# Performance work log

Hardware: AMD Instinct MI355X
Metric: run time of the kernel (lower is better)

Reference implementation:

```python
import jax, jax.numpy as jnp
import numpy as np

EPS = 1e-12  # matches torch F.normalize default eps

def setup_inputs() -> dict:
    key = jax.random.key(0)
    k1, k2 = jax.random.split(key)
    pred = jax.random.normal(k1, (32768, 2, 1024), dtype=jnp.float32)
    gt = jax.random.normal(k2, (32768, 2, 1024), dtype=jnp.float32)
    return {"pred": pred, "gt": gt}

def _l2_normalize(x):
    norm = jnp.sqrt(jnp.sum(x * x, axis=-1, keepdims=True))
    return x / jnp.maximum(norm, EPS)

def reference(pred, gt):
    # pred, gt: [B, 2, D]
    p = _l2_normalize(pred)
    g = _l2_normalize(gt)
    # cos: [B, 2, 2] cosine-similarity matrix between slots
    cos = jnp.einsum('bid,bjd->bij', p, g)
    # Hungarian assignment over a 2x2 cost (-cos) reduces to choosing the
    # larger of trace vs anti-trace of cos.
    s_id = cos[:, 0, 0] + cos[:, 1, 1]    # identity assignment sum
    s_sw = cos[:, 0, 1] + cos[:, 1, 0]    # swapped assignment sum
    # selection is done on detached values in the original (scipy on .detach())
    pick_id = jax.lax.stop_gradient(s_id >= s_sw)
    best_sum = jnp.where(pick_id, s_id, s_sw)
    loss_b = 1.0 - best_sum / 2.0          # 1 - mean of the 2 matched sims
    return jnp.mean(loss_b)
```

## Files before the change

kernel.cpp:

```cpp
#include <hip/hip_runtime.h>

#define NROWS 32768
#define DDIM 1024
#define ROWS_PER_BLOCK 16
#define ROWS_PER_WAVE 4

static __device__ __forceinline__ float dot4(float4 a, float4 b) {
    return a.x * b.x + a.y * b.y + a.z * b.z + a.w * b.w;
}

__global__ __launch_bounds__(256) void cosloss_main(const float* __restrict__ pred,
                                                    const float* __restrict__ gt,
                                                    float* __restrict__ partial) {
    const int wave = threadIdx.x >> 6;
    const int lane = threadIdx.x & 63;
    __shared__ float s_wave[4];

    float wave_best = 0.0f;
    const int row0 = blockIdx.x * ROWS_PER_BLOCK + wave * ROWS_PER_WAVE;

    for (int r = 0; r < ROWS_PER_WAVE; ++r) {
        const int row = row0 + r;
        const float4* pp = (const float4*)(pred + (size_t)row * (2 * DDIM));
        const float4* gg = (const float4*)(gt + (size_t)row * (2 * DDIM));

        float np0 = 0.f, np1 = 0.f, ng0 = 0.f, ng1 = 0.f;
        float d00 = 0.f, d01 = 0.f, d10 = 0.f, d11 = 0.f;

        #pragma unroll
        for (int k = 0; k < 4; ++k) {
            const int idx = k * 64 + lane;
            float4 a0 = pp[idx];
            float4 a1 = pp[idx + 256];
            float4 b0 = gg[idx];
            float4 b1 = gg[idx + 256];
            np0 += dot4(a0, a0);
            np1 += dot4(a1, a1);
            ng0 += dot4(b0, b0);
            ng1 += dot4(b1, b1);
            d00 += dot4(a0, b0);
            d01 += dot4(a0, b1);
            d10 += dot4(a1, b0);
            d11 += dot4(a1, b1);
        }

        #pragma unroll
        for (int off = 32; off; off >>= 1) {
            np0 += __shfl_xor(np0, off);
            np1 += __shfl_xor(np1, off);
            ng0 += __shfl_xor(ng0, off);
            ng1 += __shfl_xor(ng1, off);
            d00 += __shfl_xor(d00, off);
            d01 += __shfl_xor(d01, off);
            d10 += __shfl_xor(d10, off);
            d11 += __shfl_xor(d11, off);
        }

        if (lane == 0) {
            const float EPS = 1e-12f;
            float ip0 = 1.0f / fmaxf(sqrtf(np0), EPS);
            float ip1 = 1.0f / fmaxf(sqrtf(np1), EPS);
            float ig0 = 1.0f / fmaxf(sqrtf(ng0), EPS);
            float ig1 = 1.0f / fmaxf(sqrtf(ng1), EPS);
            float c00 = d00 * ip0 * ig0;
            float c01 = d01 * ip0 * ig1;
            float c10 = d10 * ip1 * ig0;
            float c11 = d11 * ip1 * ig1;
            float s_id = c00 + c11;
            float s_sw = c01 + c10;
            wave_best += (s_id >= s_sw) ? s_id : s_sw;
        }
    }

    if (lane == 0) s_wave[wave] = wave_best;
    __syncthreads();
    if (threadIdx.x == 0) {
        partial[blockIdx.x] = s_wave[0] + s_wave[1] + s_wave[2] + s_wave[3];
    }
}

__global__ __launch_bounds__(256) void cosloss_final(const float* __restrict__ partial,
                                                     float* __restrict__ out, int n) {
    __shared__ float s[256];
    float acc = 0.0f;
    for (int i = threadIdx.x; i < n; i += 256) acc += partial[i];
    s[threadIdx.x] = acc;
    __syncthreads();
    for (int step = 128; step; step >>= 1) {
        if (threadIdx.x < step) s[threadIdx.x] += s[threadIdx.x + step];
        __syncthreads();
    }
    if (threadIdx.x == 0) out[0] = 1.0f - s[0] / (2.0f * (float)NROWS);
}

extern "C" void kernel_launch(void* const* d_in, const int* in_sizes, int n_in,
                              void* d_out, int out_size, void* d_ws, size_t ws_size,
                              hipStream_t stream) {
    const float* pred = (const float*)d_in[0];
    const float* gt   = (const float*)d_in[1];
    float* out        = (float*)d_out;
    float* partial    = (float*)d_ws;

    const int nblocks = NROWS / ROWS_PER_BLOCK;
    cosloss_main<<<nblocks, 256, 0, stream>>>(pred, gt, partial);
    cosloss_final<<<1, 256, 0, stream>>>(partial, out, nblocks);
}
```

Baseline: 102.7 us.

## Map rows to 16-lane groups and use nontemporal loads

Each wave now processes its four rows at once, with one 16-lane group per row, instead of looping over rows with the full wave. Every lane issues sixteen iterations of four 16-byte nontemporal loads, and the shuffle reduction shrinks to four steps within each 16-lane group. The cross-row sum is done with two extra shuffles. This is meant to put more independent loads in flight per lane and to avoid polluting the cache on a pure streaming read. The trade-off is that each wave-wide load instruction now covers four separate 256-byte row segments rather than one contiguous 1 KB span.

```diff
diff --git a/kernel.cpp b/kernel.cpp
--- a/kernel.cpp
+++ b/kernel.cpp
@@ -3,10 +3,15 @@
 #define NROWS 32768
 #define DDIM 1024
 #define ROWS_PER_BLOCK 16
-#define ROWS_PER_WAVE 4
 
-static __device__ __forceinline__ float dot4(float4 a, float4 b) {
+using f32x4 = __attribute__((ext_vector_type(4))) float;
+
+static __device__ __forceinline__ float dot4(f32x4 a, f32x4 b) {
     return a.x * b.x + a.y * b.y + a.z * b.z + a.w * b.w;
+}
+
+static __device__ __forceinline__ f32x4 ntload(const f32x4* p) {
+    return __builtin_nontemporal_load(p);
 }
 
 __global__ __launch_bounds__(256) void cosloss_main(const float* __restrict__ pred,
@@ -14,65 +19,65 @@
                                                     float* __restrict__ partial) {
     const int wave = threadIdx.x >> 6;
     const int lane = threadIdx.x & 63;
+    const int grp  = lane >> 4;
+    const int sub  = lane & 15;
     __shared__ float s_wave[4];
 
-    float wave_best = 0.0f;
-    const int row0 = blockIdx.x * ROWS_PER_BLOCK + wave * ROWS_PER_WAVE;
+    const int row = blockIdx.x * ROWS_PER_BLOCK + wave * 4 + grp;
+    const f32x4* pp = (const f32x4*)(pred + (size_t)row * (2 * DDIM));
+    const f32x4* gg = (const f32x4*)(gt + (size_t)row * (2 * DDIM));
 
-    for (int r = 0; r < ROWS_PER_WAVE; ++r) {
-        const int row = row0 + r;
-        const float4* pp = (const float4*)(pred + (size_t)row * (2 * DDIM));
-        const float4* gg = (const float4*)(gt + (size_t)row * (2 * DDIM));
+    float np0 = 0.f, np1 = 0.f, ng0 = 0.f, ng1 = 0.f;
+    float d00 = 0.f, d01 = 0.f, d10 = 0.f, d11 = 0.f;
 
-        float np0 = 0.f, np1 = 0.f, ng0 = 0.f, ng1 = 0.f;
-        float d00 = 0.f, d01 = 0.f, d10 = 0.f, d11 = 0.f;
-
-        #pragma unroll
-        for (int k = 0; k < 4; ++k) {
-            const int idx = k * 64 + lane;
-            float4 a0 = pp[idx];
-            float4 a1 = pp[idx + 256];
-            float4 b0 = gg[idx];
-            float4 b1 = gg[idx + 256];
-            np0 += dot4(a0, a0);
-            np1 += dot4(a1, a1);
-            ng0 += dot4(b0, b0);
-            ng1 += dot4(b1, b1);
-            d00 += dot4(a0, b0);
-            d01 += dot4(a0, b1);
-            d10 += dot4(a1, b0);
-            d11 += dot4(a1, b1);
-        }
-
-        #pragma unroll
-        for (int off = 32; off; off >>= 1) {
-            np0 += __shfl_xor(np0, off);
-            np1 += __shfl_xor(np1, off);
-            ng0 += __shfl_xor(ng0, off);
-            ng1 += __shfl_xor(ng1, off);
-            d00 += __shfl_xor(d00, off);
-            d01 += __shfl_xor(d01, off);
-            d10 += __shfl_xor(d10, off);
-            d11 += __shfl_xor(d11, off);
-        }
-
-        if (lane == 0) {
-            const float EPS = 1e-12f;
-            float ip0 = 1.0f / fmaxf(sqrtf(np0), EPS);
-            float ip1 = 1.0f / fmaxf(sqrtf(np1), EPS);
-            float ig0 = 1.0f / fmaxf(sqrtf(ng0), EPS);
-            float ig1 = 1.0f / fmaxf(sqrtf(ng1), EPS);
-            float c00 = d00 * ip0 * ig0;
-            float c01 = d01 * ip0 * ig1;
-            float c10 = d10 * ip1 * ig0;
-            float c11 = d11 * ip1 * ig1;
-            float s_id = c00 + c11;
-            float s_sw = c01 + c10;
-            wave_best += (s_id >= s_sw) ? s_id : s_sw;
-        }
+    #pragma unroll 4
+    for (int i = 0; i < 16; ++i) {
+        const int idx = i * 16 + sub;
+        f32x4 a0 = ntload(pp + idx);
+        f32x4 a1 = ntload(pp + idx + 256);
+        f32x4 b0 = ntload(gg + idx);
+        f32x4 b1 = ntload(gg + idx + 256);
+        np0 += dot4(a0, a0);
+        np1 += dot4(a1, a1);
+        ng0 += dot4(b0, b0);
+        ng1 += dot4(b1, b1);
+        d00 += dot4(a0, b0);
+        d01 += dot4(a0, b1);
+        d10 += dot4(a1, b0);
+        d11 += dot4(a1, b1);
     }
 
-    if (lane == 0) s_wave[wave] = wave_best;
+    #pragma unroll
+    for (int off = 1; off < 16; off <<= 1) {
+        np0 += __shfl_xor(np0, off);
+        np1 += __shfl_xor(np1, off);
+        ng0 += __shfl_xor(ng0, off);
+        ng1 += __shfl_xor(ng1, off);
+        d00 += __shfl_xor(d00, off);
+        d01 += __shfl_xor(d01, off);
+        d10 += __shfl_xor(d10, off);
+        d11 += __shfl_xor(d11, off);
+    }
+
+    float best = 0.0f;
+    if (sub == 0) {
+        const float EPS = 1e-12f;
+        float ip0 = 1.0f / fmaxf(sqrtf(np0), EPS);
+        float ip1 = 1.0f / fmaxf(sqrtf(np1), EPS);
+        float ig0 = 1.0f / fmaxf(sqrtf(ng0), EPS);
+        float ig1 = 1.0f / fmaxf(sqrtf(ng1), EPS);
+        float c00 = d00 * ip0 * ig0;
+        float c01 = d01 * ip0 * ig1;
+        float c10 = d10 * ip1 * ig0;
+        float c11 = d11 * ip1 * ig1;
+        float s_id = c00 + c11;
+        float s_sw = c01 + c10;
+        best = (s_id >= s_sw) ? s_id : s_sw;
+    }
+    best += __shfl_xor(best, 16);
+    best += __shfl_xor(best, 32);
+
+    if (lane == 0) s_wave[wave] = best;
     __syncthreads();
     if (threadIdx.x == 0) {
         partial[blockIdx.x] = s_wave[0] + s_wave[1] + s_wave[2] + s_wave[3];
```

New measurement: 98.78 us. -3.8%, faster.
